# Optimization experiments

Hardware: AMD Instinct MI355X
Metric: run time of the kernel (lower is better)

Reference implementation:

```python
import jax, jax.numpy as jnp
import numpy as np

N = 50000   # nodes
E = 800000  # edges
G = 64      # graphs in the batch
DIN = 128
DOUT = 256


def _lin(key, fan_in, fan_out):
    s = 1.0 / np.sqrt(fan_in)
    kw, kb = jax.random.split(key)
    W = jax.random.uniform(kw, (fan_in, fan_out), jnp.float32, -s, s)
    b = jax.random.uniform(kb, (fan_out,), jnp.float32, -s, s)
    return W, b


def setup_inputs() -> dict:
    key = jax.random.key(0)
    ks = jax.random.split(key, 12)
    x = jax.random.normal(ks[0], (N, DIN), jnp.float32)
    edge_index = jax.random.randint(ks[1], (2, E), 0, N, dtype=jnp.int64)
    batch = jnp.sort(jax.random.randint(ks[2], (N,), 0, G, dtype=jnp.int64))
    W1, b1 = _lin(ks[3], DIN, 128)
    W2, b2 = _lin(ks[4], 128, 128)
    W3, b3 = _lin(ks[5], 128, 128)
    A1, ba1 = _lin(ks[6], DIN, 64)
    A2, ba2 = _lin(ks[7], 64, 32)
    A3, ba3 = _lin(ks[8], 32, 1)
    M1, bm1 = _lin(ks[9], 128, 128)
    M2, bm2 = _lin(ks[10], 128, DOUT)
    return dict(x=x, edge_index=edge_index, batch=batch,
                W1=W1, b1=b1, W2=W2, b2=b2, W3=W3, b3=b3,
                A1=A1, ba1=ba1, A2=A2, ba2=ba2, A3=A3, ba3=ba3,
                M1=M1, bm1=bm1, M2=M2, bm2=bm2)


def _gcn_norm(edge_index, n, dtype):
    # GCNConv default: add self-loops, symmetric normalization D^-1/2 (A+I) D^-1/2
    loop = jnp.arange(n, dtype=edge_index.dtype)
    src = jnp.concatenate([edge_index[0], loop])
    dst = jnp.concatenate([edge_index[1], loop])
    deg = jax.ops.segment_sum(jnp.ones_like(dst, dtype), dst, num_segments=n)
    dinv = jnp.where(deg > 0, jax.lax.rsqrt(deg), 0.0)
    return src, dst, dinv[src] * dinv[dst]


def _gcn(h, W, b, src, dst, norm, n):
    h = h @ W                                   # [N, F_out]
    msg = h[src] * norm[:, None]                # gather + scale (memory bound)
    return jax.ops.segment_sum(msg, dst, num_segments=n) + b


def _segment_softmax(w, batch, g):
    # per-graph softmax (PyG softmax): stabilize with segment max
    m = jax.ops.segment_max(w, batch, num_segments=g)
    e = jnp.exp(w - m[batch])
    s = jax.ops.segment_sum(e, batch, num_segments=g)
    return e / (s[batch] + 1e-16)


def reference(x, edge_index, batch,
              W1, b1, W2, b2, W3, b3,
              A1, ba1, A2, ba2, A3, ba3,
              M1, bm1, M2, bm2):
    n = x.shape[0]
    src, dst, norm = _gcn_norm(edge_index, n, x.dtype)
    relu = jax.nn.relu
    # feature branch
    f = relu(_gcn(x, W1, b1, src, dst, norm, n))
    f = relu(_gcn(f, W2, b2, src, dst, norm, n))
    f = relu(_gcn(f, W3, b3, src, dst, norm, n))
    # attention branch
    w = relu(_gcn(x, A1, ba1, src, dst, norm, n))
    w = relu(_gcn(w, A2, ba2, src, dst, norm, n))
    w = relu(_gcn(w, A3, ba3, src, dst, norm, n))   # [N, 1]
    w = _segment_softmax(w, batch, G)
    # attention-weighted sum pooling per graph
    pooled = jax.ops.segment_sum(f * w, batch, num_segments=G)  # [G, 128]
    # MLP([128,128,256], batch_norm=False): Linear+ReLU, plain last Linear
    out = relu(pooled @ M1 + bm1) @ M2 + bm2
    return out
```

## Files before the change

### kernel.cpp

```cpp
#include <hip/hip_runtime.h>
#include <hip/hip_fp16.h>
#include <math.h>


#define DIN 128
#define FH  128
#define DOUT 256
#define NBUK 128
#define SUBN 512
#define IMGCAP 16384

typedef float f4 __attribute__((ext_vector_type(4)));
typedef float f32x4 __attribute__((ext_vector_type(4)));
typedef _Float16 h8v __attribute__((ext_vector_type(8)));
typedef _Float16 h4v __attribute__((ext_vector_type(4)));


__global__ void hist_kernel(const int* __restrict__ dst, int* __restrict__ cnt, int E) {
    int e = blockIdx.x * 256 + threadIdx.x;
    if (e < E) atomicAdd(&cnt[dst[e]], 1);
}

__global__ void dinv_kernel(const int* __restrict__ cnt, float* __restrict__ dinv, int n) {
    int i = blockIdx.x * 256 + threadIdx.x;
    if (i < n) dinv[i] = rsqrtf((float)(cnt[i] + 1));
}

__global__ __launch_bounds__(256) void scan1_kernel(const int* __restrict__ cnt,
                                                    int* __restrict__ bsum, int n) {
    __shared__ int sm[256];
    int tid = threadIdx.x;
    int base = blockIdx.x * 512;
    int a = (base + tid < n) ? cnt[base + tid] : 0;
    int b = (base + 256 + tid < n) ? cnt[base + 256 + tid] : 0;
    sm[tid] = a + b;
    __syncthreads();
    for (int off = 128; off > 0; off >>= 1) {
        if (tid < off) sm[tid] += sm[tid + off];
        __syncthreads();
    }
    if (tid == 0) bsum[blockIdx.x] = sm[0];
}

__global__ void scan2_kernel(const int* __restrict__ bsum, int* __restrict__ boff,
                             int* __restrict__ rpN, int nb) {
    if (threadIdx.x == 0) {
        int run = 0;
        for (int i = 0; i < nb; ++i) { boff[i] = run; run += bsum[i]; }
        *rpN = run;
    }
}

__global__ __launch_bounds__(256) void scan3_kernel(const int* __restrict__ cnt,
        const int* __restrict__ boff, int* __restrict__ rp, int n) {
    __shared__ int sm[256];
    int tid = threadIdx.x;
    int base = blockIdx.x * 512;
    int i0 = base + 2 * tid;
    int c0 = (i0 < n) ? cnt[i0] : 0;
    int c1 = (i0 + 1 < n) ? cnt[i0 + 1] : 0;
    int ps = c0 + c1;
    sm[tid] = ps;
    __syncthreads();
    for (int off = 1; off < 256; off <<= 1) {
        int v = (tid >= off) ? sm[tid - off] : 0;
        __syncthreads();
        sm[tid] += v;
        __syncthreads();
    }
    int excl = sm[tid] - ps + boff[blockIdx.x];
    if (i0 < n) rp[i0] = excl;
    if (i0 + 1 < n) rp[i0 + 1] = excl + c0;
}

__global__ __launch_bounds__(256) void ebucket_kernel(const int* __restrict__ src,
        const int* __restrict__ dst, int* __restrict__ bcur,
        unsigned long long* __restrict__ entries, int E, int shift) {
    __shared__ int lcnt[NBUK], lbase[NBUK], lcur[NBUK];
    const int tid = threadIdx.x;
    const int e0 = blockIdx.x * 2048;
    if (tid < NBUK) lcnt[tid] = 0;
    __syncthreads();
    int s_[8], d_[8];
    #pragma unroll
    for (int k = 0; k < 8; ++k) {
        int e = e0 + k * 256 + tid;
        if (e < E) {
            s_[k] = src[e];
            d_[k] = dst[e];
            atomicAdd(&lcnt[d_[k] >> shift], 1);
        } else {
            d_[k] = -1;
        }
    }
    __syncthreads();
    if (tid < NBUK) {
        lbase[tid] = lcnt[tid] ? atomicAdd(&bcur[tid], lcnt[tid]) : 0;
        lcur[tid] = 0;
    }
    __syncthreads();
    #pragma unroll
    for (int k = 0; k < 8; ++k) {
        if (d_[k] >= 0) {
            int b = d_[k] >> shift;
            int idx = atomicAdd(&lcur[b], 1);
            entries[(size_t)(lbase[b] + idx)] =
                ((unsigned long long)(unsigned)d_[k] << 32) | (unsigned)s_[k];
        }
    }
}

__global__ __launch_bounds__(512) void ecsr_kernel(
        const unsigned long long* __restrict__ entries,
        const int* __restrict__ rp, const float* __restrict__ dinv,
        long long* __restrict__ cn, int n, int shift) {
    __shared__ long long img[IMGCAP];
    __shared__ int hist[SUBN];
    __shared__ int lcur[SUBN];
    __shared__ int sm[SUBN];
    __shared__ float dl[SUBN];
    const int b = blockIdx.x;
    const int n0 = b << shift;
    if (n0 >= n) return;
    const int n1 = min(n0 + (1 << shift), n);
    const int base = rp[n0];
    const int len  = rp[n1] - base;
    const int tid = threadIdx.x;
    hist[tid] = 0;
    lcur[tid] = 0;
    if (n0 + tid < n1) dl[tid] = dinv[n0 + tid];
    __syncthreads();
    for (int i = base + tid; i < base + len; i += 512)
        atomicAdd(&hist[(int)(entries[i] >> 32) - n0], 1);
    __syncthreads();
    int v = hist[tid];
    sm[tid] = v;
    __syncthreads();
    for (int off = 1; off < SUBN; off <<= 1) {
        int t = (tid >= off) ? sm[tid - off] : 0;
        __syncthreads();
        sm[tid] += t;
        __syncthreads();
    }
    hist[tid] = sm[tid] - v;
    __syncthreads();
    const bool fits = (len <= IMGCAP);
    for (int i = base + tid; i < base + len; i += 512) {
        unsigned long long e = entries[i];
        int d  = (int)(e >> 32) - n0;
        int sx = (int)(unsigned)(e & 0xffffffffu);
        int pos = hist[d] + atomicAdd(&lcur[d], 1);
        float w = dinv[sx] * dl[d];
        long long val = (long long)(unsigned)sx | ((long long)__float_as_int(w) << 32);
        if (fits) img[pos] = val;
        else      cn[base + pos] = val;
    }
    __syncthreads();
    if (fits)
        for (int i = tid; i < len; i += 512) cn[base + i] = img[i];
}

__global__ void gstart_kernel(const int* __restrict__ batch, int* __restrict__ gstart,
                              const int* __restrict__ rp, int* __restrict__ bcur,
                              int n, int g, int shift) {
    int t = threadIdx.x;
    if (t < NBUK) bcur[t] = rp[min(t << shift, n)];
    if (t > g) return;
    int lo = 0, hi = n;
    while (lo < hi) {
        int mid = (lo + hi) >> 1;
        if (batch[mid] < t) lo = mid + 1; else hi = mid;
    }
    gstart[t] = lo;
}

__global__ void cvt16_kernel(const float* __restrict__ in, __half* __restrict__ outh,
                             long n8) {
    long i = (long)blockIdx.x * 256 + threadIdx.x;
    if (i >= n8) return;
    f4 a = ((const f4*)in)[2 * i];
    f4 b = ((const f4*)in)[2 * i + 1];
    __half2 h0 = __float22half2_rn(make_float2(a.x, a.y));
    __half2 h1 = __float22half2_rn(make_float2(a.z, a.w));
    __half2 h2 = __float22half2_rn(make_float2(b.x, b.y));
    __half2 h3 = __float22half2_rn(make_float2(b.z, b.w));
    uint4 st;
    st.x = *(unsigned*)&h0; st.y = *(unsigned*)&h1;
    st.z = *(unsigned*)&h2; st.w = *(unsigned*)&h3;
    ((uint4*)outh)[i] = st;
}


__device__ __forceinline__ void wsplit(const float* __restrict__ W,
        _Float16* __restrict__ Th, _Float16* __restrict__ Tl,
        int fin, int fout, int i) {
    int r = i / fout, c = i % fout;
    float w = W[i];
    _Float16 h = (_Float16)w;
    Th[c * fin + r] = h;
    Tl[c * fin + r] = (_Float16)(w - (float)h);
}

__global__ __launch_bounds__(256) void wprep_kernel(const float* __restrict__ W1,
        const float* __restrict__ W2, const float* __restrict__ W3,
        const float* __restrict__ A1, const float* __restrict__ A2,
        _Float16* __restrict__ T) {
    int i = blockIdx.x * 256 + threadIdx.x;
    if (i < 16384)       wsplit(W1, T,          T + 16384,  128, 128, i);
    else if (i < 32768)  wsplit(W2, T + 32768,  T + 49152,  128, 128, i - 16384);
    else if (i < 49152)  wsplit(W3, T + 65536,  T + 81920,  128, 128, i - 32768);
    else if (i < 57344)  wsplit(A1, T + 98304,  T + 106496, 128, 64,  i - 49152);
    else if (i < 59392)  wsplit(A2, T + 114688, T + 116736, 64,  32,  i - 57344);
}


template<int FIN, int FOUT, int OMODE>
__global__ __launch_bounds__(256) void mgemm_kernel(const float* __restrict__ A,
        const _Float16* __restrict__ Wh, const _Float16* __restrict__ Wl,
        const float* __restrict__ bias, void* __restrict__ Cv, int n) {
    constexpr int NWC  = (FOUT / 16 < 4) ? FOUT / 16 : 4;
    constexpr int NWR  = 4 / NWC;
    constexpr int BM   = 64 * NWR;
    constexpr int CT   = FOUT / 16 / NWC;
    constexpr int KS   = FIN / 32;
    constexpr int LSTR = FIN + 8;
    __shared__ _Float16 Ahs[BM * LSTR];
    __shared__ _Float16 Als[BM * LSTR];

    const int tid  = threadIdx.x;
    const int w    = tid >> 6;
    const int lane = tid & 63;
    const long row0 = (long)blockIdx.x * BM;

    for (int i = tid; i < BM * (FIN / 4); i += 256) {
        int r  = i / (FIN / 4);
        int c4 = i % (FIN / 4);
        long gr = row0 + r;
        float4 v = {0.f, 0.f, 0.f, 0.f};
        if (gr < n) v = *(const float4*)&A[gr * FIN + c4 * 4];
        _Float16 h0 = (_Float16)v.x, h1 = (_Float16)v.y;
        _Float16 h2 = (_Float16)v.z, h3 = (_Float16)v.w;
        h4v hh = {h0, h1, h2, h3};
        h4v ll = {(_Float16)(v.x - (float)h0), (_Float16)(v.y - (float)h1),
                  (_Float16)(v.z - (float)h2), (_Float16)(v.w - (float)h3)};
        *(h4v*)&Ahs[r * LSTR + c4 * 4] = hh;
        *(h4v*)&Als[r * LSTR + c4 * 4] = ll;
    }

    const int wc = w % NWC;
    const int wr = w / NWC;
    const int colbase = wc * CT * 16;
    const int bk = (lane >> 4) * 8;
    h8v Bh[CT][KS], Bl[CT][KS];
    #pragma unroll
    for (int ct = 0; ct < CT; ++ct) {
        int c = colbase + ct * 16 + (lane & 15);
        #pragma unroll
        for (int kk = 0; kk < KS; ++kk) {
            Bh[ct][kk] = *(const h8v*)&Wh[(size_t)c * FIN + kk * 32 + bk];
            Bl[ct][kk] = *(const h8v*)&Wl[(size_t)c * FIN + kk * 32 + bk];
        }
    }

    __syncthreads();

    f32x4 acc[4][CT];
    #pragma unroll
    for (int rt = 0; rt < 4; ++rt)
        #pragma unroll
        for (int ct = 0; ct < CT; ++ct)
            acc[rt][ct] = (f32x4){0.f, 0.f, 0.f, 0.f};

    #pragma unroll
    for (int rt = 0; rt < 4; ++rt) {
        const int r = wr * 64 + rt * 16 + (lane & 15);
        #pragma unroll
        for (int kk = 0; kk < KS; ++kk) {
            h8v ah = *(const h8v*)&Ahs[r * LSTR + kk * 32 + bk];
            h8v al = *(const h8v*)&Als[r * LSTR + kk * 32 + bk];
            #pragma unroll
            for (int ct = 0; ct < CT; ++ct) {
                acc[rt][ct] = __builtin_amdgcn_mfma_f32_16x16x32_f16(
                    ah, Bh[ct][kk], acc[rt][ct], 0, 0, 0);
                acc[rt][ct] = __builtin_amdgcn_mfma_f32_16x16x32_f16(
                    ah, Bl[ct][kk], acc[rt][ct], 0, 0, 0);
                acc[rt][ct] = __builtin_amdgcn_mfma_f32_16x16x32_f16(
                    al, Bh[ct][kk], acc[rt][ct], 0, 0, 0);
            }
        }
    }

    #pragma unroll
    for (int rt = 0; rt < 4; ++rt) {
        const long rbase = row0 + wr * 64 + rt * 16 + (lane >> 4) * 4;
        #pragma unroll
        for (int ct = 0; ct < CT; ++ct) {
            const int col = colbase + ct * 16 + (lane & 15);
            if (OMODE == 1) {
                const float bv = bias[col];
                #pragma unroll
                for (int j = 0; j < 4; ++j) {
                    long r = rbase + j;
                    if (r < n)
                        ((float*)Cv)[r * FOUT + col] = fmaxf(acc[rt][ct][j] + bv, 0.f);
                }
            } else {
                #pragma unroll
                for (int j = 0; j < 4; ++j) {
                    long r = rbase + j;
                    if (r < n)
                        ((__half*)Cv)[r * FOUT + col] = __float2half(acc[rt][ct][j]);
                }
            }
        }
    }
}

__global__ void a3_kernel(const float* __restrict__ A, const float* __restrict__ W,
                          float* __restrict__ out, int n) {
    int i = blockIdx.x * 256 + threadIdx.x;
    if (i >= n) return;
    const float4* a = (const float4*)(A + (size_t)i * 32);
    float acc = 0.f;
    #pragma unroll
    for (int q = 0; q < 8; ++q) {
        float4 v = a[q];
        float4 w = ((const float4*)W)[q];
        acc += v.x * w.x + v.y * w.y + v.z * w.z + v.w * w.w;
    }
    out[i] = acc;
}


__device__ __forceinline__ void hacc8(float acc[8], uint4 u, float w) {
    __half2 h; float2 f;
    h = *(__half2*)&u.x; f = __half22float2(h); acc[0] += w * f.x; acc[1] += w * f.y;
    h = *(__half2*)&u.y; f = __half22float2(h); acc[2] += w * f.x; acc[3] += w * f.y;
    h = *(__half2*)&u.z; f = __half22float2(h); acc[4] += w * f.x; acc[5] += w * f.y;
    h = *(__half2*)&u.w; f = __half22float2(h); acc[6] += w * f.x; acc[7] += w * f.y;
}

template<int F, bool BR>
__global__ __launch_bounds__(256) void aggh_kernel(const __half* __restrict__ tin,
        const float* __restrict__ bias, const float* __restrict__ dinv,
        const int* __restrict__ rp, const long long* __restrict__ cn,
        float* __restrict__ out, int n) {
    constexpr int LPR   = F / 8;
    constexpr int SLOTS = 64 / LPR;
    const int lane = threadIdx.x & 63;
    const int node = blockIdx.x * 4 + (threadIdx.x >> 6);
    if (node >= n) return;
    const int l    = lane % LPR;
    const int slot = lane / LPR;
    const uint4* base = (const uint4*)tin + l;
    const int e0 = rp[node], e1 = rp[node + 1];
    float acc[8] = {0.f, 0.f, 0.f, 0.f, 0.f, 0.f, 0.f, 0.f};
    if (slot == 0) {
        float di = dinv[node];
        uint4 u = base[(size_t)node * LPR];
        hacc8(acc, u, di * di);
    }
    int p = e0 + slot;
    for (; p + 3 * SLOTS < e1; p += 4 * SLOTS) {
        long long r0 = __builtin_nontemporal_load(cn + p);
        long long r1 = __builtin_nontemporal_load(cn + p + SLOTS);
        long long r2 = __builtin_nontemporal_load(cn + p + 2 * SLOTS);
        long long r3 = __builtin_nontemporal_load(cn + p + 3 * SLOTS);
        uint4 u0 = base[(size_t)(unsigned)r0 * LPR];
        uint4 u1 = base[(size_t)(unsigned)r1 * LPR];
        uint4 u2 = base[(size_t)(unsigned)r2 * LPR];
        uint4 u3 = base[(size_t)(unsigned)r3 * LPR];
        hacc8(acc, u0, __int_as_float((int)(r0 >> 32)));
        hacc8(acc, u1, __int_as_float((int)(r1 >> 32)));
        hacc8(acc, u2, __int_as_float((int)(r2 >> 32)));
        hacc8(acc, u3, __int_as_float((int)(r3 >> 32)));
    }
    for (; p + SLOTS < e1; p += 2 * SLOTS) {
        long long r0 = __builtin_nontemporal_load(cn + p);
        long long r1 = __builtin_nontemporal_load(cn + p + SLOTS);
        uint4 u0 = base[(size_t)(unsigned)r0 * LPR];
        uint4 u1 = base[(size_t)(unsigned)r1 * LPR];
        hacc8(acc, u0, __int_as_float((int)(r0 >> 32)));
        hacc8(acc, u1, __int_as_float((int)(r1 >> 32)));
    }
    if (p < e1) {
        long long r0 = __builtin_nontemporal_load(cn + p);
        uint4 u0 = base[(size_t)(unsigned)r0 * LPR];
        hacc8(acc, u0, __int_as_float((int)(r0 >> 32)));
    }
    #pragma unroll
    for (int off = 32; off >= LPR; off >>= 1) {
        #pragma unroll
        for (int j = 0; j < 8; ++j) acc[j] += __shfl_xor(acc[j], off);
    }
    if (slot == 0) {
        if (BR) {
            #pragma unroll
            for (int j = 0; j < 8; ++j)
                acc[j] = fmaxf(acc[j] + bias[l * 8 + j], 0.f);
        }
        f4 lo = {acc[0], acc[1], acc[2], acc[3]};
        f4 hi = {acc[4], acc[5], acc[6], acc[7]};
        float* o = out + (size_t)node * F + l * 8;
        __builtin_nontemporal_store(lo, (f4*)o);
        __builtin_nontemporal_store(hi, (f4*)(o + 4));
    }
}

__global__ void agg1_kernel(const float* __restrict__ tin, const float* __restrict__ bias,
        const float* __restrict__ dinv, const int* __restrict__ rp,
        const long long* __restrict__ cn, float* __restrict__ out, int n) {
    int i = blockIdx.x * 256 + threadIdx.x;
    if (i >= n) return;
    float di = dinv[i];
    float acc = di * di * tin[i];
    int e0 = rp[i], e1 = rp[i + 1];
    int p = e0;
    float a0 = 0.f, a1 = 0.f, a2 = 0.f, a3 = 0.f;
    for (; p + 3 < e1; p += 4) {
        long long r0 = __builtin_nontemporal_load(cn + p);
        long long r1 = __builtin_nontemporal_load(cn + p + 1);
        long long r2 = __builtin_nontemporal_load(cn + p + 2);
        long long r3 = __builtin_nontemporal_load(cn + p + 3);
        a0 += __int_as_float((int)(r0 >> 32)) * tin[(int)(unsigned)r0];
        a1 += __int_as_float((int)(r1 >> 32)) * tin[(int)(unsigned)r1];
        a2 += __int_as_float((int)(r2 >> 32)) * tin[(int)(unsigned)r2];
        a3 += __int_as_float((int)(r3 >> 32)) * tin[(int)(unsigned)r3];
    }
    for (; p < e1; ++p) {
        long long r0 = __builtin_nontemporal_load(cn + p);
        a0 += __int_as_float((int)(r0 >> 32)) * tin[(int)(unsigned)r0];
    }
    acc += a0 + a1 + a2 + a3 + bias[0];
    out[i] = acc > 0.f ? acc : 0.f;
}


__global__ __launch_bounds__(256) void smexp_kernel(const float* __restrict__ w,
        const int* __restrict__ gstart, float* __restrict__ gsum,
        float* __restrict__ e) {
    const int g = blockIdx.x;
    const int a = gstart[g], b = gstart[g + 1];
    const int tid = threadIdx.x;
    __shared__ float red[4];
    float m = 0.f;
    for (int i = a + tid; i < b; i += 256) m = fmaxf(m, w[i]);
    #pragma unroll
    for (int off = 32; off > 0; off >>= 1) m = fmaxf(m, __shfl_xor(m, off));
    if ((tid & 63) == 0) red[tid >> 6] = m;
    __syncthreads();
    m = fmaxf(fmaxf(red[0], red[1]), fmaxf(red[2], red[3]));
    float s = 0.f;
    for (int i = a + tid; i < b; i += 256) {
        float ex = expf(w[i] - m);
        e[i] = ex;
        s += ex;
    }
    #pragma unroll
    for (int off = 32; off > 0; off >>= 1) s += __shfl_xor(s, off);
    __syncthreads();
    if ((tid & 63) == 0) red[tid >> 6] = s;
    __syncthreads();
    if (tid == 0) gsum[g] = red[0] + red[1] + red[2] + red[3];
}


__global__ __launch_bounds__(128) void pool_kernel(const float* __restrict__ f3,
        const float* __restrict__ e, const float* __restrict__ gsum,
        const int* __restrict__ gstart, float* __restrict__ pooled) {
    constexpr int SPG = 64;
    const int g = blockIdx.x / SPG, s = blockIdx.x % SPG;
    const int a = gstart[g], bnd = gstart[g + 1];
    const int len = bnd - a;
    if (len <= 0) return;
    const int chunk = (len + SPG - 1) / SPG;
    const int lo = a + s * chunk;
    const int hi = min(lo + chunk, bnd);
    if (lo >= hi) return;
    const float inv = 1.f / (gsum[g] + 1e-16f);
    const int tid = threadIdx.x;
    const int lane4 = tid & 31;
    const int rs    = tid >> 5;
    f4 acc = {0.f, 0.f, 0.f, 0.f};
    for (int i = lo + rs; i < hi; i += 4) {
        float w = e[i] * inv;
        f4 v = *(const f4*)&f3[(size_t)i * FH + lane4 * 4];
        acc.x += w * v.x; acc.y += w * v.y;
        acc.z += w * v.z; acc.w += w * v.w;
    }
    acc.x += __shfl_xor(acc.x, 32);
    acc.y += __shfl_xor(acc.y, 32);
    acc.z += __shfl_xor(acc.z, 32);
    acc.w += __shfl_xor(acc.w, 32);
    __shared__ float sm[128];
    if (tid >= 64 && tid < 96) *(f4*)&sm[(tid - 64) * 4] = acc;
    __syncthreads();
    if (tid < 32) {
        f4 o = *(f4*)&sm[tid * 4];
        o.x += acc.x; o.y += acc.y; o.z += acc.z; o.w += acc.w;
        float* dst = &pooled[g * FH + tid * 4];
        atomicAdd(dst + 0, o.x);
        atomicAdd(dst + 1, o.y);
        atomicAdd(dst + 2, o.z);
        atomicAdd(dst + 3, o.w);
    }
}


__global__ __launch_bounds__(128) void mlp1_kernel(const float* __restrict__ pooled,
        const float* __restrict__ M1, const float* __restrict__ bm1,
        float* __restrict__ hidden) {
    __shared__ float pr[FH];
    int g = blockIdx.x, j = threadIdx.x;
    pr[j] = pooled[g * FH + j];
    __syncthreads();
    float acc = bm1[j];
    #pragma unroll 8
    for (int k = 0; k < FH; ++k) acc += pr[k] * M1[k * FH + j];
    hidden[g * FH + j] = acc > 0.f ? acc : 0.f;
}

__global__ __launch_bounds__(256) void mlp2_kernel(const float* __restrict__ hidden,
        const float* __restrict__ M2, const float* __restrict__ bm2,
        float* __restrict__ out) {
    __shared__ float hr[FH];
    int g = blockIdx.x, j = threadIdx.x;
    if (j < FH) hr[j] = hidden[g * FH + j];
    __syncthreads();
    float acc = bm2[j];
    #pragma unroll 8
    for (int k = 0; k < FH; ++k) acc += hr[k] * M2[k * DOUT + j];
    out[g * DOUT + j] = acc;
}


extern "C" void kernel_launch(void* const* d_in, const int* in_sizes, int n_in,
                              void* d_out, int out_size, void* d_ws, size_t ws_size,
                              hipStream_t stream) {
    const float* x   = (const float*)d_in[0];
    const int*   ei  = (const int*)d_in[1];
    const int*   batch = (const int*)d_in[2];
    const float* W1  = (const float*)d_in[3];
    const float* b1  = (const float*)d_in[4];
    const float* W2  = (const float*)d_in[5];
    const float* b2  = (const float*)d_in[6];
    const float* W3  = (const float*)d_in[7];
    const float* b3  = (const float*)d_in[8];
    const float* A1  = (const float*)d_in[9];
    const float* ba1 = (const float*)d_in[10];
    const float* A2  = (const float*)d_in[11];
    const float* ba2 = (const float*)d_in[12];
    const float* A3  = (const float*)d_in[13];
    const float* ba3 = (const float*)d_in[14];
    const float* M1  = (const float*)d_in[15];
    const float* bm1 = (const float*)d_in[16];
    const float* M2  = (const float*)d_in[17];
    const float* bm2 = (const float*)d_in[18];

    const int N = in_sizes[0] / DIN;
    const int E = in_sizes[1] / 2;
    const int G = out_size / DOUT;
    const int* src = ei;
    const int* dst = ei + E;
    float* out = (float*)d_out;

    int shift = 9;
    while (((N + (1 << shift) - 1) >> shift) > NBUK) ++shift;
    const int nbuckets = (N + (1 << shift) - 1) >> shift;

    char* p = (char*)d_ws;
    auto alloc = [&](size_t bytes) -> void* {
        void* r = (void*)p;
        p += (bytes + 255) & ~(size_t)255;
        return r;
    };
    float* dinv  = (float*)alloc((size_t)N * 4);
    int*   cnt   = (int*)alloc((size_t)N * 4);
    int*   rp    = (int*)alloc((size_t)(N + 1) * 4);
    long long* cn = (long long*)alloc((size_t)E * 8);
    float* SY    = (float*)alloc((size_t)N * FH * 4);
    float* SA    = (float*)alloc((size_t)N * FH * 4);
    __half* ST   = (__half*)alloc((size_t)N * FH * 2);
    char*  SX    = (char*)alloc((size_t)N * 256);
    __half* u2   = (__half*)alloc((size_t)N * 32 * 2);
    float* a2    = (float*)alloc((size_t)N * 32 * 4);
    float* wlin  = (float*)alloc((size_t)N * 4);
    float* wact  = (float*)alloc((size_t)N * 4);
    float* ebuf  = (float*)alloc((size_t)N * 4);
    float* gsum  = (float*)alloc((size_t)G * 4);
    int*   gstart= (int*)alloc((size_t)(G + 1) * 4);
    float* pooled= (float*)alloc((size_t)G * FH * 4);
    float* hidden= (float*)alloc((size_t)G * FH * 4);
    int*   bsum  = (int*)alloc(256 * 4);
    int*   boff  = (int*)alloc(256 * 4);
    int*   bcur  = (int*)alloc(NBUK * 4);
    _Float16* WT = (_Float16*)alloc((size_t)118784 * 2);

    __half* xh = (__half*)SX;
    float*  a1 = (float*)SX;
    unsigned long long* entries = (unsigned long long*)SA;

    hipMemsetAsync(cnt, 0, (size_t)N * 4, stream);
    hipMemsetAsync(pooled, 0, (size_t)G * FH * 4, stream);

    const int eb = (E + 255) / 256;
    const int nb = (N + 255) / 256;
    const int NB = (N + 511) / 512;

    wprep_kernel<<<232, 256, 0, stream>>>(W1, W2, W3, A1, A2, WT);
    hist_kernel<<<eb, 256, 0, stream>>>(dst, cnt, E);
    dinv_kernel<<<nb, 256, 0, stream>>>(cnt, dinv, N);
    scan1_kernel<<<NB, 256, 0, stream>>>(cnt, bsum, N);
    scan2_kernel<<<1, 64, 0, stream>>>(bsum, boff, rp + N, NB);
    scan3_kernel<<<NB, 256, 0, stream>>>(cnt, boff, rp, N);
    gstart_kernel<<<1, 128, 0, stream>>>(batch, gstart, rp, bcur, N, G, shift);

    ebucket_kernel<<<(E + 2047) / 2048, 256, 0, stream>>>(src, dst, bcur, entries, E, shift);
    ecsr_kernel<<<nbuckets, 512, 0, stream>>>(entries, rp, dinv, cn, N, shift);

    const long n8 = (long)N * FH / 8;
    cvt16_kernel<<<(int)((n8 + 255) / 256), 256, 0, stream>>>(x, xh, n8);

    const int gb64  = (N + 63) / 64;
    const int gb128 = (N + 127) / 128;
    const int agb = (N + 3) / 4;

    aggh_kernel<FH, false><<<agb, 256, 0, stream>>>(xh, nullptr, dinv, rp, cn, SY, N);

    mgemm_kernel<FH, FH, 1><<<gb64, 256, 0, stream>>>(SY, WT, WT + 16384, b1, SA, N);
    mgemm_kernel<FH, 64, 1><<<gb64, 256, 0, stream>>>(SY, WT + 98304, WT + 106496, ba1, a1, N);

    mgemm_kernel<FH, FH, 2><<<gb64, 256, 0, stream>>>(SA, WT + 32768, WT + 49152, nullptr, ST, N);
    aggh_kernel<FH, true><<<agb, 256, 0, stream>>>(ST, b2, dinv, rp, cn, SA, N);
    mgemm_kernel<FH, FH, 2><<<gb64, 256, 0, stream>>>(SA, WT + 65536, WT + 81920, nullptr, ST, N);
    aggh_kernel<FH, true><<<agb, 256, 0, stream>>>(ST, b3, dinv, rp, cn, SY, N);

    mgemm_kernel<64, 32, 2><<<gb128, 256, 0, stream>>>(a1, WT + 114688, WT + 116736, nullptr, u2, N);
    aggh_kernel<32, true><<<agb, 256, 0, stream>>>(u2, ba2, dinv, rp, cn, a2, N);
    a3_kernel<<<nb, 256, 0, stream>>>(a2, A3, wlin, N);
    agg1_kernel<<<nb, 256, 0, stream>>>(wlin, ba3, dinv, rp, cn, wact, N);

    smexp_kernel<<<G, 256, 0, stream>>>(wact, gstart, gsum, ebuf);
    pool_kernel<<<G * 64, 128, 0, stream>>>(SY, ebuf, gsum, gstart, pooled);

    mlp1_kernel<<<G, 128, 0, stream>>>(pooled, M1, bm1, hidden);
    mlp2_kernel<<<G, 256, 0, stream>>>(hidden, M2, bm2, out);
}
```

Measured before the change: 361.5 us.

## Fuse layer-1 GEMMs with attention GEMMs and merge degree histogram into bucketing

Runs the layer-1 feature GEMM, the layer-2 feature GEMM, A1 and A2 together in one kernel that keeps intermediates in LDS, so the SA/a1 round-trips through global memory go away. The second attention aggregation now also applies the A3 dot product, which removes a3_kernel and the a2 buffer. The degree histogram moves into ebucket and dinv into scan1, and buckets get fixed ECAP-sized slots so bucketing no longer waits for the scan. The fixed slots silently drop edges if a bucket overflows ECAP, and the fused kernel's large LDS footprint may lower occupancy.

```diff
diff --git a/kernel.cpp b/kernel.cpp
--- a/kernel.cpp
+++ b/kernel.cpp
@@ -9,6 +9,7 @@
 #define NBUK 128
 #define SUBN 512
 #define IMGCAP 16384
+#define ECAP 16384
 
 typedef float f4 __attribute__((ext_vector_type(4)));
 typedef float f32x4 __attribute__((ext_vector_type(4)));
@@ -16,23 +17,15 @@
 typedef _Float16 h4v __attribute__((ext_vector_type(4)));
 
 
-__global__ void hist_kernel(const int* __restrict__ dst, int* __restrict__ cnt, int E) {
-    int e = blockIdx.x * 256 + threadIdx.x;
-    if (e < E) atomicAdd(&cnt[dst[e]], 1);
-}
-
-__global__ void dinv_kernel(const int* __restrict__ cnt, float* __restrict__ dinv, int n) {
-    int i = blockIdx.x * 256 + threadIdx.x;
-    if (i < n) dinv[i] = rsqrtf((float)(cnt[i] + 1));
-}
-
 __global__ __launch_bounds__(256) void scan1_kernel(const int* __restrict__ cnt,
-                                                    int* __restrict__ bsum, int n) {
+        int* __restrict__ bsum, float* __restrict__ dinv, int n) {
     __shared__ int sm[256];
     int tid = threadIdx.x;
     int base = blockIdx.x * 512;
     int a = (base + tid < n) ? cnt[base + tid] : 0;
     int b = (base + 256 + tid < n) ? cnt[base + 256 + tid] : 0;
+    if (base + tid < n)       dinv[base + tid]       = rsqrtf((float)(a + 1));
+    if (base + 256 + tid < n) dinv[base + 256 + tid] = rsqrtf((float)(b + 1));
     sm[tid] = a + b;
     __syncthreads();
     for (int off = 128; off > 0; off >>= 1) {
@@ -75,7 +68,8 @@
 
 __global__ __launch_bounds__(256) void ebucket_kernel(const int* __restrict__ src,
         const int* __restrict__ dst, int* __restrict__ bcur,
-        unsigned long long* __restrict__ entries, int E, int shift) {
+        unsigned long long* __restrict__ entries, int* __restrict__ cnt,
+        int E, int shift) {
     __shared__ int lcnt[NBUK], lbase[NBUK], lcur[NBUK];
     const int tid = threadIdx.x;
     const int e0 = blockIdx.x * 2048;
@@ -89,6 +83,7 @@
             s_[k] = src[e];
             d_[k] = dst[e];
             atomicAdd(&lcnt[d_[k] >> shift], 1);
+            atomicAdd(&cnt[d_[k]], 1);
         } else {
             d_[k] = -1;
         }
@@ -103,9 +98,10 @@
     for (int k = 0; k < 8; ++k) {
         if (d_[k] >= 0) {
             int b = d_[k] >> shift;
-            int idx = atomicAdd(&lcur[b], 1);
-            entries[(size_t)(lbase[b] + idx)] =
-                ((unsigned long long)(unsigned)d_[k] << 32) | (unsigned)s_[k];
+            int idx = lbase[b] + atomicAdd(&lcur[b], 1);
+            if (idx < (b + 1) * ECAP)
+                entries[(size_t)idx] =
+                    ((unsigned long long)(unsigned)d_[k] << 32) | (unsigned)s_[k];
         }
     }
 }
@@ -125,13 +121,14 @@
     const int n1 = min(n0 + (1 << shift), n);
     const int base = rp[n0];
     const int len  = rp[n1] - base;
+    const size_t ebase = (size_t)b * ECAP;
     const int tid = threadIdx.x;
     hist[tid] = 0;
     lcur[tid] = 0;
     if (n0 + tid < n1) dl[tid] = dinv[n0 + tid];
     __syncthreads();
-    for (int i = base + tid; i < base + len; i += 512)
-        atomicAdd(&hist[(int)(entries[i] >> 32) - n0], 1);
+    for (int i = tid; i < len; i += 512)
+        atomicAdd(&hist[(int)(entries[ebase + i] >> 32) - n0], 1);
     __syncthreads();
     int v = hist[tid];
     sm[tid] = v;
@@ -145,8 +142,8 @@
     hist[tid] = sm[tid] - v;
     __syncthreads();
     const bool fits = (len <= IMGCAP);
-    for (int i = base + tid; i < base + len; i += 512) {
-        unsigned long long e = entries[i];
+    for (int i = tid; i < len; i += 512) {
+        unsigned long long e = entries[ebase + i];
         int d  = (int)(e >> 32) - n0;
         int sx = (int)(unsigned)(e & 0xffffffffu);
         int pos = hist[d] + atomicAdd(&lcur[d], 1);
@@ -161,10 +158,8 @@
 }
 
 __global__ void gstart_kernel(const int* __restrict__ batch, int* __restrict__ gstart,
-                              const int* __restrict__ rp, int* __restrict__ bcur,
-                              int n, int g, int shift) {
+                              int n, int g) {
     int t = threadIdx.x;
-    if (t < NBUK) bcur[t] = rp[min(t << shift, n)];
     if (t > g) return;
     int lo = 0, hi = n;
     while (lo < hi) {
@@ -204,8 +199,9 @@
 __global__ __launch_bounds__(256) void wprep_kernel(const float* __restrict__ W1,
         const float* __restrict__ W2, const float* __restrict__ W3,
         const float* __restrict__ A1, const float* __restrict__ A2,
-        _Float16* __restrict__ T) {
+        _Float16* __restrict__ T, int* __restrict__ bcur) {
     int i = blockIdx.x * 256 + threadIdx.x;
+    if (blockIdx.x == 0 && threadIdx.x < NBUK) bcur[threadIdx.x] = threadIdx.x * ECAP;
     if (i < 16384)       wsplit(W1, T,          T + 16384,  128, 128, i);
     else if (i < 32768)  wsplit(W2, T + 32768,  T + 49152,  128, 128, i - 16384);
     else if (i < 49152)  wsplit(W3, T + 65536,  T + 81920,  128, 128, i - 32768);
@@ -213,6 +209,213 @@
     else if (i < 59392)  wsplit(A2, T + 114688, T + 116736, 64,  32,  i - 57344);
 }
 
+
+__global__ __launch_bounds__(256) void fusedl1_kernel(const float* __restrict__ Y,
+        const _Float16* __restrict__ T, const float* __restrict__ b1,
+        const float* __restrict__ ba1, __half* __restrict__ t2,
+        __half* __restrict__ u2, int n) {
+    constexpr int LSTR  = 136;
+    constexpr int LSTRB = 72;
+    __shared__ _Float16 Yh[64 * LSTR], Yl[64 * LSTR];
+    __shared__ _Float16 Fh[64 * LSTR], Fl[64 * LSTR];
+    const int tid  = threadIdx.x;
+    const int w    = tid >> 6;
+    const int lane = tid & 63;
+    const int bk   = (lane >> 4) * 8;
+    const int cl   = lane & 15;
+    const long row0 = (long)blockIdx.x * 64;
+
+    for (int i = tid; i < 64 * 32; i += 256) {
+        int r = i >> 5, c4 = i & 31;
+        long gr = row0 + r;
+        float4 v = {0.f, 0.f, 0.f, 0.f};
+        if (gr < n) v = *(const float4*)&Y[gr * 128 + c4 * 4];
+        _Float16 h0 = (_Float16)v.x, h1 = (_Float16)v.y;
+        _Float16 h2 = (_Float16)v.z, h3 = (_Float16)v.w;
+        *(h4v*)&Yh[r * LSTR + c4 * 4] = (h4v){h0, h1, h2, h3};
+        *(h4v*)&Yl[r * LSTR + c4 * 4] =
+            (h4v){(_Float16)(v.x - (float)h0), (_Float16)(v.y - (float)h1),
+                  (_Float16)(v.z - (float)h2), (_Float16)(v.w - (float)h3)};
+    }
+    __syncthreads();
+
+    {
+        const _Float16* W1h = T;
+        const _Float16* W1l = T + 16384;
+        h8v Bh[2][4], Bl[2][4];
+        #pragma unroll
+        for (int ct = 0; ct < 2; ++ct) {
+            int c = w * 32 + ct * 16 + cl;
+            #pragma unroll
+            for (int kk = 0; kk < 4; ++kk) {
+                Bh[ct][kk] = *(const h8v*)&W1h[c * 128 + kk * 32 + bk];
+                Bl[ct][kk] = *(const h8v*)&W1l[c * 128 + kk * 32 + bk];
+            }
+        }
+        f32x4 acc[4][2];
+        #pragma unroll
+        for (int rt = 0; rt < 4; ++rt)
+            #pragma unroll
+            for (int ct = 0; ct < 2; ++ct) acc[rt][ct] = (f32x4){0.f,0.f,0.f,0.f};
+        #pragma unroll
+        for (int rt = 0; rt < 4; ++rt) {
+            int r = rt * 16 + cl;
+            #pragma unroll
+            for (int kk = 0; kk < 4; ++kk) {
+                h8v ah = *(const h8v*)&Yh[r * LSTR + kk * 32 + bk];
+                h8v al = *(const h8v*)&Yl[r * LSTR + kk * 32 + bk];
+                #pragma unroll
+                for (int ct = 0; ct < 2; ++ct) {
+                    acc[rt][ct] = __builtin_amdgcn_mfma_f32_16x16x32_f16(ah, Bh[ct][kk], acc[rt][ct], 0, 0, 0);
+                    acc[rt][ct] = __builtin_amdgcn_mfma_f32_16x16x32_f16(ah, Bl[ct][kk], acc[rt][ct], 0, 0, 0);
+                    acc[rt][ct] = __builtin_amdgcn_mfma_f32_16x16x32_f16(al, Bh[ct][kk], acc[rt][ct], 0, 0, 0);
+                }
+            }
+        }
+        #pragma unroll
+        for (int rt = 0; rt < 4; ++rt) {
+            int rowb = rt * 16 + (lane >> 4) * 4;
+            #pragma unroll
+            for (int ct = 0; ct < 2; ++ct) {
+                int col = w * 32 + ct * 16 + cl;
+                float bv = b1[col];
+                #pragma unroll
+                for (int j = 0; j < 4; ++j) {
+                    float v = fmaxf(acc[rt][ct][j] + bv, 0.f);
+                    _Float16 h = (_Float16)v;
+                    Fh[(rowb + j) * LSTR + col] = h;
+                    Fl[(rowb + j) * LSTR + col] = (_Float16)(v - (float)h);
+                }
+            }
+        }
+    }
+    __syncthreads();
+
+    {
+        const _Float16* W2h = T + 32768;
+        const _Float16* W2l = T + 49152;
+        h8v Bh[2][4], Bl[2][4];
+        #pragma unroll
+        for (int ct = 0; ct < 2; ++ct) {
+            int c = w * 32 + ct * 16 + cl;
+            #pragma unroll
+            for (int kk = 0; kk < 4; ++kk) {
+                Bh[ct][kk] = *(const h8v*)&W2h[c * 128 + kk * 32 + bk];
+                Bl[ct][kk] = *(const h8v*)&W2l[c * 128 + kk * 32 + bk];
+            }
+        }
+        f32x4 acc[4][2];
+        #pragma unroll
+        for (int rt = 0; rt < 4; ++rt)
+            #pragma unroll
+            for (int ct = 0; ct < 2; ++ct) acc[rt][ct] = (f32x4){0.f,0.f,0.f,0.f};
+        #pragma unroll
+        for (int rt = 0; rt < 4; ++rt) {
+            int r = rt * 16 + cl;
+            #pragma unroll
+            for (int kk = 0; kk < 4; ++kk) {
+                h8v ah = *(const h8v*)&Fh[r * LSTR + kk * 32 + bk];
+                h8v al = *(const h8v*)&Fl[r * LSTR + kk * 32 + bk];
+                #pragma unroll
+                for (int ct = 0; ct < 2; ++ct) {
+                    acc[rt][ct] = __builtin_amdgcn_mfma_f32_16x16x32_f16(ah, Bh[ct][kk], acc[rt][ct], 0, 0, 0);
+                    acc[rt][ct] = __builtin_amdgcn_mfma_f32_16x16x32_f16(ah, Bl[ct][kk], acc[rt][ct], 0, 0, 0);
+                    acc[rt][ct] = __builtin_amdgcn_mfma_f32_16x16x32_f16(al, Bh[ct][kk], acc[rt][ct], 0, 0, 0);
+                }
+            }
+        }
+        __syncthreads();
+        #pragma unroll
+        for (int rt = 0; rt < 4; ++rt) {
+            long rbase = row0 + rt * 16 + (lane >> 4) * 4;
+            #pragma unroll
+            for (int ct = 0; ct < 2; ++ct) {
+                int col = w * 32 + ct * 16 + cl;
+                #pragma unroll
+                for (int j = 0; j < 4; ++j) {
+                    long r = rbase + j;
+                    if (r < n) t2[r * 128 + col] = __float2half(acc[rt][ct][j]);
+                }
+            }
+        }
+    }
+
+    {
+        const _Float16* A1h = T + 98304;
+        const _Float16* A1l = T + 106496;
+        int c = w * 16 + cl;
+        h8v Bh[4], Bl[4];
+        #pragma unroll
+        for (int kk = 0; kk < 4; ++kk) {
+            Bh[kk] = *(const h8v*)&A1h[c * 128 + kk * 32 + bk];
+            Bl[kk] = *(const h8v*)&A1l[c * 128 + kk * 32 + bk];
+        }
+        f32x4 acc[4];
+        #pragma unroll
+        for (int rt = 0; rt < 4; ++rt) acc[rt] = (f32x4){0.f,0.f,0.f,0.f};
+        #pragma unroll
+        for (int rt = 0; rt < 4; ++rt) {
+            int r = rt * 16 + cl;
+            #pragma unroll
+            for (int kk = 0; kk < 4; ++kk) {
+                h8v ah = *(const h8v*)&Yh[r * LSTR + kk * 32 + bk];
+                h8v al = *(const h8v*)&Yl[r * LSTR + kk * 32 + bk];
+                acc[rt] = __builtin_amdgcn_mfma_f32_16x16x32_f16(ah, Bh[kk], acc[rt], 0, 0, 0);
+                acc[rt] = __builtin_amdgcn_mfma_f32_16x16x32_f16(ah, Bl[kk], acc[rt], 0, 0, 0);
+                acc[rt] = __builtin_amdgcn_mfma_f32_16x16x32_f16(al, Bh[kk], acc[rt], 0, 0, 0);
+            }
+        }
+        float bv = ba1[c];
+        #pragma unroll
+        for (int rt = 0; rt < 4; ++rt) {
+            int rowb = rt * 16 + (lane >> 4) * 4;
+            #pragma unroll
+            for (int j = 0; j < 4; ++j) {
+                float v = fmaxf(acc[rt][j] + bv, 0.f);
+                _Float16 h = (_Float16)v;
+                Fh[(rowb + j) * LSTRB + c] = h;
+                Fl[(rowb + j) * LSTRB + c] = (_Float16)(v - (float)h);
+            }
+        }
+    }
+    __syncthreads();
+
+    if (w < 2) {
+        const _Float16* A2h = T + 114688;
+        const _Float16* A2l = T + 116736;
+        int c = w * 16 + cl;
+        h8v Bh[2], Bl[2];
+        #pragma unroll
+        for (int kk = 0; kk < 2; ++kk) {
+            Bh[kk] = *(const h8v*)&A2h[c * 64 + kk * 32 + bk];
+            Bl[kk] = *(const h8v*)&A2l[c * 64 + kk * 32 + bk];
+        }
+        f32x4 acc[4];
+        #pragma unroll
+        for (int rt = 0; rt < 4; ++rt) acc[rt] = (f32x4){0.f,0.f,0.f,0.f};
+        #pragma unroll
+        for (int rt = 0; rt < 4; ++rt) {
+            int r = rt * 16 + cl;
+            #pragma unroll
+            for (int kk = 0; kk < 2; ++kk) {
+                h8v ah = *(const h8v*)&Fh[r * LSTRB + kk * 32 + bk];
+                h8v al = *(const h8v*)&Fl[r * LSTRB + kk * 32 + bk];
+                acc[rt] = __builtin_amdgcn_mfma_f32_16x16x32_f16(ah, Bh[kk], acc[rt], 0, 0, 0);
+                acc[rt] = __builtin_amdgcn_mfma_f32_16x16x32_f16(ah, Bl[kk], acc[rt], 0, 0, 0);
+                acc[rt] = __builtin_amdgcn_mfma_f32_16x16x32_f16(al, Bh[kk], acc[rt], 0, 0, 0);
+            }
+        }
+        #pragma unroll
+        for (int rt = 0; rt < 4; ++rt) {
+            long rbase = row0 + rt * 16 + (lane >> 4) * 4;
+            #pragma unroll
+            for (int j = 0; j < 4; ++j) {
+                long r = rbase + j;
+                if (r < n) u2[r * 32 + c] = __float2half(acc[rt][j]);
+            }
+        }
+    }
+}
 
 template<int FIN, int FOUT, int OMODE>
 __global__ __launch_bounds__(256) void mgemm_kernel(const float* __restrict__ A,
@@ -280,12 +483,9 @@
             h8v al = *(const h8v*)&Als[r * LSTR + kk * 32 + bk];
             #pragma unroll
             for (int ct = 0; ct < CT; ++ct) {
-                acc[rt][ct] = __builtin_amdgcn_mfma_f32_16x16x32_f16(
-                    ah, Bh[ct][kk], acc[rt][ct], 0, 0, 0);
-                acc[rt][ct] = __builtin_amdgcn_mfma_f32_16x16x32_f16(
-                    ah, Bl[ct][kk], acc[rt][ct], 0, 0, 0);
-                acc[rt][ct] = __builtin_amdgcn_mfma_f32_16x16x32_f16(
-                    al, Bh[ct][kk], acc[rt][ct], 0, 0, 0);
+                acc[rt][ct] = __builtin_amdgcn_mfma_f32_16x16x32_f16(ah, Bh[ct][kk], acc[rt][ct], 0, 0, 0);
+                acc[rt][ct] = __builtin_amdgcn_mfma_f32_16x16x32_f16(ah, Bl[ct][kk], acc[rt][ct], 0, 0, 0);
+                acc[rt][ct] = __builtin_amdgcn_mfma_f32_16x16x32_f16(al, Bh[ct][kk], acc[rt][ct], 0, 0, 0);
             }
         }
     }
@@ -314,21 +514,6 @@
             }
         }
     }
-}
-
-__global__ void a3_kernel(const float* __restrict__ A, const float* __restrict__ W,
-                          float* __restrict__ out, int n) {
-    int i = blockIdx.x * 256 + threadIdx.x;
-    if (i >= n) return;
-    const float4* a = (const float4*)(A + (size_t)i * 32);
-    float acc = 0.f;
-    #pragma unroll
-    for (int q = 0; q < 8; ++q) {
-        float4 v = a[q];
-        float4 w = ((const float4*)W)[q];
-        acc += v.x * w.x + v.y * w.y + v.z * w.z + v.w * w.w;
-    }
-    out[i] = acc;
 }
 
 
@@ -404,6 +589,55 @@
         float* o = out + (size_t)node * F + l * 8;
         __builtin_nontemporal_store(lo, (f4*)o);
         __builtin_nontemporal_store(hi, (f4*)(o + 4));
+    }
+}
+
+__global__ __launch_bounds__(256) void aggh32a_kernel(const __half* __restrict__ tin,
+        const float* __restrict__ ba2, const float* __restrict__ A3,
+        const float* __restrict__ dinv, const int* __restrict__ rp,
+        const long long* __restrict__ cn, float* __restrict__ wlin, int n) {
+    constexpr int LPR   = 4;
+    constexpr int SLOTS = 16;
+    const int lane = threadIdx.x & 63;
+    const int node = blockIdx.x * 4 + (threadIdx.x >> 6);
+    if (node >= n) return;
+    const int l    = lane % LPR;
+    const int slot = lane / LPR;
+    const uint4* base = (const uint4*)tin + l;
+    const int e0 = rp[node], e1 = rp[node + 1];
+    float acc[8] = {0.f, 0.f, 0.f, 0.f, 0.f, 0.f, 0.f, 0.f};
+    if (slot == 0) {
+        float di = dinv[node];
+        uint4 u = base[(size_t)node * LPR];
+        hacc8(acc, u, di * di);
+    }
+    int p = e0 + slot;
+    for (; p + SLOTS < e1; p += 2 * SLOTS) {
+        long long r0 = __builtin_nontemporal_load(cn + p);
+        long long r1 = __builtin_nontemporal_load(cn + p + SLOTS);
+        uint4 u0 = base[(size_t)(unsigned)r0 * LPR];
+        uint4 u1 = base[(size_t)(unsigned)r1 * LPR];
+        hacc8(acc, u0, __int_as_float((int)(r0 >> 32)));
+        hacc8(acc, u1, __int_as_float((int)(r1 >> 32)));
+    }
+    if (p < e1) {
+        long long r0 = __builtin_nontemporal_load(cn + p);
+        uint4 u0 = base[(size_t)(unsigned)r0 * LPR];
+        hacc8(acc, u0, __int_as_float((int)(r0 >> 32)));
+    }
+    #pragma unroll
+    for (int off = 32; off >= LPR; off >>= 1) {
+        #pragma unroll
+        for (int j = 0; j < 8; ++j) acc[j] += __shfl_xor(acc[j], off);
+    }
+    if (slot == 0) {
+        float part = 0.f;
+        #pragma unroll
+        for (int j = 0; j < 8; ++j)
+            part += fmaxf(acc[j] + ba2[l * 8 + j], 0.f) * A3[l * 8 + j];
+        part += __shfl_xor(part, 1);
+        part += __shfl_xor(part, 2);
+        if (l == 0) wlin[node] = part;
     }
 }
 
@@ -583,7 +817,6 @@
     __half* ST   = (__half*)alloc((size_t)N * FH * 2);
     char*  SX    = (char*)alloc((size_t)N * 256);
     __half* u2   = (__half*)alloc((size_t)N * 32 * 2);
-    float* a2    = (float*)alloc((size_t)N * 32 * 4);
     float* wlin  = (float*)alloc((size_t)N * 4);
     float* wact  = (float*)alloc((size_t)N * 4);
     float* ebuf  = (float*)alloc((size_t)N * 4);
@@ -597,47 +830,37 @@
     _Float16* WT = (_Float16*)alloc((size_t)118784 * 2);
 
     __half* xh = (__half*)SX;
-    float*  a1 = (float*)SX;
     unsigned long long* entries = (unsigned long long*)SA;
 
     hipMemsetAsync(cnt, 0, (size_t)N * 4, stream);
     hipMemsetAsync(pooled, 0, (size_t)G * FH * 4, stream);
 
-    const int eb = (E + 255) / 256;
     const int nb = (N + 255) / 256;
     const int NB = (N + 511) / 512;
 
-    wprep_kernel<<<232, 256, 0, stream>>>(W1, W2, W3, A1, A2, WT);
-    hist_kernel<<<eb, 256, 0, stream>>>(dst, cnt, E);
-    dinv_kernel<<<nb, 256, 0, stream>>>(cnt, dinv, N);
-    scan1_kernel<<<NB, 256, 0, stream>>>(cnt, bsum, N);
+    wprep_kernel<<<232, 256, 0, stream>>>(W1, W2, W3, A1, A2, WT, bcur);
+    ebucket_kernel<<<(E + 2047) / 2048, 256, 0, stream>>>(src, dst, bcur, entries, cnt, E, shift);
+    scan1_kernel<<<NB, 256, 0, stream>>>(cnt, bsum, dinv, N);
     scan2_kernel<<<1, 64, 0, stream>>>(bsum, boff, rp + N, NB);
     scan3_kernel<<<NB, 256, 0, stream>>>(cnt, boff, rp, N);
-    gstart_kernel<<<1, 128, 0, stream>>>(batch, gstart, rp, bcur, N, G, shift);
-
-    ebucket_kernel<<<(E + 2047) / 2048, 256, 0, stream>>>(src, dst, bcur, entries, E, shift);
+    gstart_kernel<<<1, 128, 0, stream>>>(batch, gstart, N, G);
     ecsr_kernel<<<nbuckets, 512, 0, stream>>>(entries, rp, dinv, cn, N, shift);
 
     const long n8 = (long)N * FH / 8;
     cvt16_kernel<<<(int)((n8 + 255) / 256), 256, 0, stream>>>(x, xh, n8);
 
-    const int gb64  = (N + 63) / 64;
-    const int gb128 = (N + 127) / 128;
-    const int agb = (N + 3) / 4;
+    const int gb64 = (N + 63) / 64;
+    const int agb  = (N + 3) / 4;
 
     aggh_kernel<FH, false><<<agb, 256, 0, stream>>>(xh, nullptr, dinv, rp, cn, SY, N);
 
-    mgemm_kernel<FH, FH, 1><<<gb64, 256, 0, stream>>>(SY, WT, WT + 16384, b1, SA, N);
-    mgemm_kernel<FH, 64, 1><<<gb64, 256, 0, stream>>>(SY, WT + 98304, WT + 106496, ba1, a1, N);
-
-    mgemm_kernel<FH, FH, 2><<<gb64, 256, 0, stream>>>(SA, WT + 32768, WT + 49152, nullptr, ST, N);
+    fusedl1_kernel<<<gb64, 256, 0, stream>>>(SY, WT, b1, ba1, (__half*)ST, u2, N);
+
     aggh_kernel<FH, true><<<agb, 256, 0, stream>>>(ST, b2, dinv, rp, cn, SA, N);
     mgemm_kernel<FH, FH, 2><<<gb64, 256, 0, stream>>>(SA, WT + 65536, WT + 81920, nullptr, ST, N);
     aggh_kernel<FH, true><<<agb, 256, 0, stream>>>(ST, b3, dinv, rp, cn, SY, N);
 
-    mgemm_kernel<64, 32, 2><<<gb128, 256, 0, stream>>>(a1, WT + 114688, WT + 116736, nullptr, u2, N);
-    aggh_kernel<32, true><<<agb, 256, 0, stream>>>(u2, ba2, dinv, rp, cn, a2, N);
-    a3_kernel<<<nb, 256, 0, stream>>>(a2, A3, wlin, N);
+    aggh32a_kernel<<<agb, 256, 0, stream>>>(u2, ba2, A3, dinv, rp, cn, wlin, N);
     agg1_kernel<<<nb, 256, 0, stream>>>(wlin, ba3, dinv, rp, cn, wact, N);
 
     smexp_kernel<<<G, 256, 0, stream>>>(wact, gstart, gsum, ebuf);
```

After: 332.7 us. 8.0% less time.
